# Performance work log

Measured on AMD Instinct MI355X. Metric: run time of the kernel, lower is better.

Reference implementation:

```python
import jax, jax.numpy as jnp
import numpy as np

N_NODES = 50000
N_EDGES = 1600000
E_DIM = 128
N_LAYERS = 3
N_GRAPHS = 32


def setup_inputs() -> dict:
    key = jax.random.key(0)
    ks = jax.random.split(key, 12)
    x = jax.random.normal(ks[0], (N_NODES,), dtype=jnp.float32)
    edge_index = jax.random.randint(ks[1], (2, N_EDGES), 0, N_NODES, dtype=jnp.int32)
    batch = jnp.sort(jax.random.randint(ks[2], (N_NODES,), 0, N_GRAPHS, dtype=jnp.int32))
    s_in = 1.0  # fan_in = 1 for the first linear
    s_e = 1.0 / np.sqrt(E_DIM)
    lin_w = jax.random.normal(ks[3], (1, E_DIM), jnp.float32) * s_in
    lin_b = jax.random.normal(ks[4], (E_DIM,), jnp.float32) * 0.01
    gcn_w = jax.random.normal(ks[5], (N_LAYERS, E_DIM, E_DIM), jnp.float32) * s_e
    gcn_b = jax.random.normal(ks[6], (N_LAYERS, E_DIM), jnp.float32) * 0.01
    r1_w = jax.random.normal(ks[7], (E_DIM, E_DIM), jnp.float32) * s_e
    r1_b = jax.random.normal(ks[8], (E_DIM,), jnp.float32) * 0.01
    r2_w = jax.random.normal(ks[9], (E_DIM, 1), jnp.float32) * s_e
    r2_b = jax.random.normal(ks[10], (1,), jnp.float32) * 0.01
    return {"x": x, "edge_index": edge_index, "batch": batch,
            "lin_w": lin_w, "lin_b": lin_b, "gcn_w": gcn_w, "gcn_b": gcn_b,
            "r1_w": r1_w, "r1_b": r1_b, "r2_w": r2_w, "r2_b": r2_b}


def reference(x, edge_index, batch, lin_w, lin_b, gcn_w, gcn_b, r1_w, r1_b, r2_w, r2_b):
    # input embedding: x.view(-1, 1) @ W + b -> [N, E]
    h = x.reshape(-1, 1) @ lin_w + lin_b

    # GCN normalization (add self-loops, symmetric deg^-1/2 norm) — structure is
    # identical across layers, so compute once.
    loops = jnp.arange(N_NODES, dtype=edge_index.dtype)
    src = jnp.concatenate([edge_index[0], loops])
    dst = jnp.concatenate([edge_index[1], loops])
    deg = jax.ops.segment_sum(jnp.ones(src.shape[0], h.dtype), dst, num_segments=N_NODES)
    dinv = jnp.where(deg > 0, jax.lax.rsqrt(deg), 0.0)
    norm = (dinv[src] * dinv[dst])[:, None]  # [E+N, 1]

    # NOTE: original calls x.relu() without assignment -> no activation (faithful).
    for l in range(N_LAYERS):
        h = h @ gcn_w[l]                                        # [N, E]
        h = jax.ops.segment_sum(h[src] * norm, dst, num_segments=N_NODES) + gcn_b[l]

    # global_add_pool over graphs
    pooled = jax.ops.segment_sum(h, batch, num_segments=N_GRAPHS)  # [G, E]
    hr = jnp.tanh(pooled @ r1_w + r1_b)
    return hr @ r2_w + r2_b  # [G, 1]
```

## Files before the change

kernel.cpp:

```cpp
#include <hip/hip_runtime.h>
#include <hip/hip_bf16.h>
#include <math.h>

#define NGRAPH 32
#define CAP 10240
#define EPT 24
#define EPB (256 * EPT)

__global__ void k_part(const int* __restrict__ src, const int* __restrict__ dst,
                       int* __restrict__ gcursor, unsigned int* __restrict__ packed, int E) {
    __shared__ unsigned int ldsbuf[EPB];
    __shared__ int hist[256], lofs[256], lcur[256], base[256];
    int tid = threadIdx.x;
    int e0 = blockIdx.x * EPB;
    hist[tid] = 0;
    __syncthreads();
    int d[EPT], s[EPT];
#pragma unroll
    for (int c = 0; c < EPT / 4; c++) {
        int e = e0 + c * 1024 + (tid << 2);
        if (e + 3 < E) {
            int4 dv = *(const int4*)&dst[e];
            int4 sv = *(const int4*)&src[e];
            d[4*c+0] = dv.x; d[4*c+1] = dv.y; d[4*c+2] = dv.z; d[4*c+3] = dv.w;
            s[4*c+0] = sv.x; s[4*c+1] = sv.y; s[4*c+2] = sv.z; s[4*c+3] = sv.w;
            atomicAdd(&hist[dv.x >> 8], 1);
            atomicAdd(&hist[dv.y >> 8], 1);
            atomicAdd(&hist[dv.z >> 8], 1);
            atomicAdd(&hist[dv.w >> 8], 1);
        } else {
#pragma unroll
            for (int k = 0; k < 4; k++) {
                int ee = e + k;
                if (ee < E) {
                    d[4*c+k] = dst[ee]; s[4*c+k] = src[ee];
                    atomicAdd(&hist[d[4*c+k] >> 8], 1);
                } else {
                    d[4*c+k] = -1;
                }
            }
        }
    }
    __syncthreads();
    int v = hist[tid];
    lofs[tid] = v;
    __syncthreads();
    for (int off = 1; off < 256; off <<= 1) {
        int t = (tid >= off) ? lofs[tid - off] : 0;
        __syncthreads();
        lofs[tid] += t;
        __syncthreads();
    }
    int total = lofs[255];
    int excl = lofs[tid] - v;
    lofs[tid] = excl;
    lcur[tid] = excl;
    if (v > 0) base[tid] = tid * CAP + atomicAdd(&gcursor[tid], v);
    __syncthreads();
#pragma unroll
    for (int c = 0; c < EPT; c++) {
        int dd = d[c];
        if (dd >= 0) {
            int bk = dd >> 8;
            int slot = atomicAdd(&lcur[bk], 1);
            ldsbuf[slot] = ((unsigned int)bk << 24) | ((unsigned int)s[c] << 8)
                         | (unsigned int)(dd & 255);
        }
    }
    __syncthreads();
    for (int i = tid; i < total; i += 256) {
        unsigned int w = ldsbuf[i];
        int bk = w >> 24;
        packed[base[bk] + (i - lofs[bk])] = w & 0xFFFFFFu;
    }
}

__global__ void k_bucket(const unsigned int* __restrict__ packed, const int* __restrict__ gcursor,
                         const float* __restrict__ x, const int* __restrict__ batch,
                         int* __restrict__ offs, int* __restrict__ deg,
                         float* __restrict__ dinv, float2* __restrict__ q0,
                         unsigned short* __restrict__ csr, float* __restrict__ S, int N) {
    __shared__ int cnt[256], lofs[256], lcur[256];
    __shared__ float cs[NGRAPH];
    int tid = threadIdx.x;
    int b = blockIdx.x;
    int start = b * CAP;
    int end = start + gcursor[b];
    cnt[tid] = 0;
    if (tid < NGRAPH) cs[tid] = 0.f;
    __syncthreads();
    for (int e = start + tid; e < end; e += 256)
        atomicAdd(&cnt[packed[e] & 255], 1);
    __syncthreads();
    int v = cnt[tid];
    lofs[tid] = v;
    __syncthreads();
    for (int off = 1; off < 256; off <<= 1) {
        int t = (tid >= off) ? lofs[tid - off] : 0;
        __syncthreads();
        lofs[tid] += t;
        __syncthreads();
    }
    int excl = lofs[tid] - v;
    lcur[tid] = excl;
    int node = b * 256 + tid;
    if (node < N) {
        deg[node] = v;
        offs[node] = start + excl;
        float dv = rsqrtf((float)(v + 1));
        dinv[node] = dv;
        q0[node] = make_float2(x[node] * dv, dv);
        atomicAdd(&cs[batch[node]], 1.f);
    }
    __syncthreads();
    for (int e = start + tid; e < end; e += 256) {
        unsigned int p = packed[e];
        int pos = start + atomicAdd(&lcur[p & 255], 1);
        csr[pos] = (unsigned short)(p >> 8);
    }
    if (tid < NGRAPH && cs[tid] != 0.f) atomicAdd(&S[tid], cs[tid]);
}

template <int WRITE_Q>
__global__ void k_hop(const float2* __restrict__ qin, float2* __restrict__ pout,
                      float2* __restrict__ qout, const unsigned short* __restrict__ csr,
                      const int* __restrict__ offs, const int* __restrict__ deg,
                      const float* __restrict__ dinv, int N) {
    int tid = threadIdx.x;
    int lane = tid & 15;
    int node = blockIdx.x * 16 + (tid >> 4);
    if (node >= N) return;
    int e = offs[node], ne = deg[node];
    float sx = 0.0f, su = 0.0f;
    int j = lane;
    for (; j + 16 < ne; j += 32) {
        int i0 = csr[e + j];
        int i1 = csr[e + j + 16];
        float2 a = qin[i0];
        float2 b = qin[i1];
        sx += a.x + b.x;
        su += a.y + b.y;
    }
    if (j < ne) {
        float2 a = qin[csr[e + j]];
        sx += a.x; su += a.y;
    }
#pragma unroll
    for (int m = 8; m > 0; m >>= 1) {
        sx += __shfl_xor(sx, m);
        su += __shfl_xor(su, m);
    }
    if (lane == 0) {
        float2 qs = qin[node];
        float dv = dinv[node];
        float px = dv * (sx + qs.x), pu = dv * (su + qs.y);
        pout[node] = make_float2(px, pu);
        if (WRITE_Q) qout[node] = make_float2(px * dv, pu * dv);
    }
}

__global__ void k_sums(const float2* __restrict__ p1, const float2* __restrict__ p2,
                       const float2* __restrict__ p3, const int* __restrict__ batch,
                       float* __restrict__ S, int N) {
    __shared__ float bins[4 * NGRAPH];
    int tid = threadIdx.x;
    if (tid < 4 * NGRAPH) bins[tid] = 0.f;
    __syncthreads();
    int i = blockIdx.x * 256 + tid;
    if (i < N) {
        int g = batch[i];
        atomicAdd(&bins[g], p1[i].y);
        atomicAdd(&bins[32 + g], p2[i].y);
        atomicAdd(&bins[64 + g], p3[i].y);
        atomicAdd(&bins[96 + g], p3[i].x);
    }
    __syncthreads();
    if (tid < 4 * NGRAPH && bins[tid] != 0.f) atomicAdd(&S[32 + tid], bins[tid]);
}

__global__ void k_mlp(const float* __restrict__ S,
                      const float* __restrict__ lin_w, const float* __restrict__ lin_b,
                      const float* __restrict__ gcn_w, const float* __restrict__ gcn_b,
                      const float* __restrict__ r1_w, const float* __restrict__ r1_b,
                      const float* __restrict__ r2_w, const float* __restrict__ r2_b,
                      float* __restrict__ out) {
    __shared__ float va[128], vb[128], vc[128], vd[128], pl[128], red[128];
    int j = threadIdx.x;
    int g = blockIdx.x;
    va[j] = lin_w[j];
    vb[j] = lin_b[j];
    vc[j] = gcn_b[j];
    vd[j] = gcn_b[128 + j];
    __syncthreads();
    for (int l = 0; l < 3; l++) {
        const float* W = gcn_w + l * 128 * 128;
        float na = 0.f, nb = 0.f, nc = 0.f, nd = 0.f;
        for (int k = 0; k < 128; k++) {
            float w = W[k * 128 + j];
            na += va[k] * w;
            nb += vb[k] * w;
            nc += vc[k] * w;
            nd += vd[k] * w;
        }
        __syncthreads();
        va[j] = na; vb[j] = nb;
        if (l >= 1) vc[j] = nc;
        if (l >= 2) vd[j] = nd;
        __syncthreads();
    }
    float cnt = S[g], su1 = S[32 + g], su2 = S[64 + g], su3 = S[96 + g], sv3 = S[128 + g];
    const float* b3 = gcn_b + 2 * 128;
    pl[j] = sv3 * va[j] + su3 * vb[j] + su2 * vc[j] + su1 * vd[j] + cnt * b3[j];
    __syncthreads();
    float acc = r1_b[j];
#pragma unroll 4
    for (int k = 0; k < 128; k++) acc += pl[k] * r1_w[k * 128 + j];
    red[j] = tanhf(acc) * r2_w[j];
    __syncthreads();
    for (int sft = 64; sft > 0; sft >>= 1) {
        if (j < sft) red[j] += red[j + sft];
        __syncthreads();
    }
    if (j == 0) out[g] = red[0] + r2_b[0];
}

extern "C" void kernel_launch(void* const* d_in, const int* in_sizes, int n_in,
                              void* d_out, int out_size, void* d_ws, size_t ws_size,
                              hipStream_t stream) {
    const float* x     = (const float*)d_in[0];
    const int*   eidx  = (const int*)d_in[1];
    const int*   batch = (const int*)d_in[2];
    const float* lin_w = (const float*)d_in[3];
    const float* lin_b = (const float*)d_in[4];
    const float* gcn_w = (const float*)d_in[5];
    const float* gcn_b = (const float*)d_in[6];
    const float* r1_w  = (const float*)d_in[7];
    const float* r1_b  = (const float*)d_in[8];
    const float* r2_w  = (const float*)d_in[9];
    const float* r2_b  = (const float*)d_in[10];

    const int N = in_sizes[0];
    const int E = in_sizes[1] / 2;
    const int* src = eidx;
    const int* dst = eidx + E;
    const int NB = (N + 255) / 256;

    char* w = (char*)d_ws;
    float2* q0      = (float2*)w; w += (size_t)N * 8;
    float2* q1      = (float2*)w; w += (size_t)N * 8;
    float2* q2      = (float2*)w; w += (size_t)N * 8;
    float2* p1      = (float2*)w; w += (size_t)N * 8;
    float2* p2      = (float2*)w; w += (size_t)N * 8;
    float2* p3      = (float2*)w; w += (size_t)N * 8;
    unsigned int* packed = (unsigned int*)w; w += (size_t)256 * CAP * 4;
    int*    offs    = (int*)w;    w += (size_t)N * 4;
    int*    deg     = (int*)w;    w += (size_t)N * 4;
    float*  dinv    = (float*)w;  w += (size_t)N * 4;
    int*    gcursor = (int*)w;    w += 256 * 4;
    float*  S       = (float*)w;  w += 160 * 4;
    unsigned short* csr = (unsigned short*)w; w += (size_t)256 * CAP * 2;

    hipMemsetAsync(gcursor, 0, 256 * 4 + 160 * 4, stream);

    k_part<<<(E + EPB - 1) / EPB, 256, 0, stream>>>(src, dst, gcursor, packed, E);
    k_bucket<<<NB, 256, 0, stream>>>(packed, gcursor, x, batch, offs, deg, dinv, q0, csr, S, N);

    int hop_blocks = (N + 15) / 16;
    k_hop<1><<<hop_blocks, 256, 0, stream>>>(q0, p1, q1, csr, offs, deg, dinv, N);
    k_hop<1><<<hop_blocks, 256, 0, stream>>>(q1, p2, q2, csr, offs, deg, dinv, N);
    k_hop<0><<<hop_blocks, 256, 0, stream>>>(q2, p3, (float2*)nullptr, csr, offs, deg, dinv, N);

    k_sums<<<NB, 256, 0, stream>>>(p1, p2, p3, batch, S, N);
    k_mlp<<<NGRAPH, 128, 0, stream>>>(S, lin_w, lin_b, gcn_w, gcn_b,
                                      r1_w, r1_b, r2_w, r2_b, (float*)d_out);
}
```

Measured before the change: 173.2 us.

## Fuse all stages into one cooperative persistent kernel with grid syncs

Replaces the seven separate launches and the memset with a single cooperative kernel of 256 blocks of 1024 threads, using grid.sync between phases. The CSR build is dropped: each hop reads bucketed packed edges directly and accumulates into per-node LDS slots with shared atomics. Per-graph pooling sums are folded into the hop phases, so the separate sums pass and the p buffers disappear. This removes launch gaps and the CSR scatter, but it adds grid-wide barriers, LDS atomic contention, and the risk of occupancy limits on cooperative launch with large blocks.

```diff
diff --git a/kernel.cpp b/kernel.cpp
--- a/kernel.cpp
+++ b/kernel.cpp
@@ -1,227 +1,221 @@
 #include <hip/hip_runtime.h>
-#include <hip/hip_bf16.h>
+#include <hip/hip_cooperative_groups.h>
 #include <math.h>
+
+namespace cg = cooperative_groups;
 
 #define NGRAPH 32
 #define CAP 10240
-#define EPT 24
-#define EPB (256 * EPT)
-
-__global__ void k_part(const int* __restrict__ src, const int* __restrict__ dst,
-                       int* __restrict__ gcursor, unsigned int* __restrict__ packed, int E) {
+#define BT 1024
+#define EPT 8
+#define EPB (BT * EPT)
+
+__global__ __launch_bounds__(BT, 4) void k_fused(
+    const int* __restrict__ src, const int* __restrict__ dst,
+    const float* __restrict__ x, const int* __restrict__ batch,
+    const float* __restrict__ lin_w, const float* __restrict__ lin_b,
+    const float* __restrict__ gcn_w, const float* __restrict__ gcn_b,
+    const float* __restrict__ r1_w, const float* __restrict__ r1_b,
+    const float* __restrict__ r2_w, const float* __restrict__ r2_b,
+    float* __restrict__ out,
+    unsigned int* __restrict__ packed, float* __restrict__ dinv,
+    float2* __restrict__ q0, float2* __restrict__ q1, float2* __restrict__ q2,
+    int* __restrict__ gcursor, float* __restrict__ S,
+    int N, int E)
+{
+    cg::grid_group grid = cg::this_grid();
     __shared__ unsigned int ldsbuf[EPB];
-    __shared__ int hist[256], lofs[256], lcur[256], base[256];
-    int tid = threadIdx.x;
-    int e0 = blockIdx.x * EPB;
-    hist[tid] = 0;
-    __syncthreads();
-    int d[EPT], s[EPT];
-#pragma unroll
-    for (int c = 0; c < EPT / 4; c++) {
-        int e = e0 + c * 1024 + (tid << 2);
-        if (e + 3 < E) {
-            int4 dv = *(const int4*)&dst[e];
-            int4 sv = *(const int4*)&src[e];
-            d[4*c+0] = dv.x; d[4*c+1] = dv.y; d[4*c+2] = dv.z; d[4*c+3] = dv.w;
-            s[4*c+0] = sv.x; s[4*c+1] = sv.y; s[4*c+2] = sv.z; s[4*c+3] = sv.w;
-            atomicAdd(&hist[dv.x >> 8], 1);
-            atomicAdd(&hist[dv.y >> 8], 1);
-            atomicAdd(&hist[dv.z >> 8], 1);
-            atomicAdd(&hist[dv.w >> 8], 1);
-        } else {
-#pragma unroll
-            for (int k = 0; k < 4; k++) {
-                int ee = e + k;
-                if (ee < E) {
-                    d[4*c+k] = dst[ee]; s[4*c+k] = src[ee];
-                    atomicAdd(&hist[d[4*c+k] >> 8], 1);
-                } else {
-                    d[4*c+k] = -1;
+    __shared__ int hist[256], lofs[256], lcur[256], basearr[256];
+    __shared__ float accx[256], accu[256];
+    __shared__ float bins[3 * NGRAPH];
+    __shared__ float va[128], vb[128], vc[128], vd[128], pl[128], red[128];
+
+    const int tid = threadIdx.x;
+    const int b = blockIdx.x;
+    const int NB = (N + 255) >> 8;
+    const int ntiles = (E + EPB - 1) / EPB;
+
+    if (b == 0) {
+        if (tid < 256) gcursor[tid] = 0;
+        else if (tid < 256 + 160) S[tid - 256] = 0.f;
+    }
+    grid.sync();
+
+    if (b < ntiles) {
+        int e0 = b * EPB;
+        if (tid < 256) hist[tid] = 0;
+        __syncthreads();
+        int dA[EPT], sA[EPT];
+#pragma unroll
+        for (int c = 0; c < EPT / 4; c++) {
+            int e = e0 + c * 4096 + (tid << 2);
+            if (e + 3 < E) {
+                int4 dv4 = *(const int4*)&dst[e];
+                int4 sv4 = *(const int4*)&src[e];
+                dA[4*c+0] = dv4.x; dA[4*c+1] = dv4.y; dA[4*c+2] = dv4.z; dA[4*c+3] = dv4.w;
+                sA[4*c+0] = sv4.x; sA[4*c+1] = sv4.y; sA[4*c+2] = sv4.z; sA[4*c+3] = sv4.w;
+                atomicAdd(&hist[dv4.x >> 8], 1);
+                atomicAdd(&hist[dv4.y >> 8], 1);
+                atomicAdd(&hist[dv4.z >> 8], 1);
+                atomicAdd(&hist[dv4.w >> 8], 1);
+            } else {
+#pragma unroll
+                for (int k = 0; k < 4; k++) {
+                    int ee = e + k;
+                    if (ee < E) {
+                        dA[4*c+k] = dst[ee]; sA[4*c+k] = src[ee];
+                        atomicAdd(&hist[dA[4*c+k] >> 8], 1);
+                    } else {
+                        dA[4*c+k] = -1;
+                    }
                 }
             }
         }
-    }
-    __syncthreads();
-    int v = hist[tid];
-    lofs[tid] = v;
-    __syncthreads();
-    for (int off = 1; off < 256; off <<= 1) {
-        int t = (tid >= off) ? lofs[tid - off] : 0;
-        __syncthreads();
-        lofs[tid] += t;
-        __syncthreads();
-    }
-    int total = lofs[255];
-    int excl = lofs[tid] - v;
-    lofs[tid] = excl;
-    lcur[tid] = excl;
-    if (v > 0) base[tid] = tid * CAP + atomicAdd(&gcursor[tid], v);
-    __syncthreads();
-#pragma unroll
-    for (int c = 0; c < EPT; c++) {
-        int dd = d[c];
-        if (dd >= 0) {
-            int bk = dd >> 8;
-            int slot = atomicAdd(&lcur[bk], 1);
-            ldsbuf[slot] = ((unsigned int)bk << 24) | ((unsigned int)s[c] << 8)
-                         | (unsigned int)(dd & 255);
-        }
-    }
-    __syncthreads();
-    for (int i = tid; i < total; i += 256) {
-        unsigned int w = ldsbuf[i];
-        int bk = w >> 24;
-        packed[base[bk] + (i - lofs[bk])] = w & 0xFFFFFFu;
-    }
-}
-
-__global__ void k_bucket(const unsigned int* __restrict__ packed, const int* __restrict__ gcursor,
-                         const float* __restrict__ x, const int* __restrict__ batch,
-                         int* __restrict__ offs, int* __restrict__ deg,
-                         float* __restrict__ dinv, float2* __restrict__ q0,
-                         unsigned short* __restrict__ csr, float* __restrict__ S, int N) {
-    __shared__ int cnt[256], lofs[256], lcur[256];
-    __shared__ float cs[NGRAPH];
-    int tid = threadIdx.x;
-    int b = blockIdx.x;
-    int start = b * CAP;
-    int end = start + gcursor[b];
-    cnt[tid] = 0;
-    if (tid < NGRAPH) cs[tid] = 0.f;
-    __syncthreads();
-    for (int e = start + tid; e < end; e += 256)
-        atomicAdd(&cnt[packed[e] & 255], 1);
-    __syncthreads();
-    int v = cnt[tid];
-    lofs[tid] = v;
-    __syncthreads();
-    for (int off = 1; off < 256; off <<= 1) {
-        int t = (tid >= off) ? lofs[tid - off] : 0;
-        __syncthreads();
-        lofs[tid] += t;
-        __syncthreads();
-    }
-    int excl = lofs[tid] - v;
-    lcur[tid] = excl;
-    int node = b * 256 + tid;
-    if (node < N) {
-        deg[node] = v;
-        offs[node] = start + excl;
-        float dv = rsqrtf((float)(v + 1));
-        dinv[node] = dv;
-        q0[node] = make_float2(x[node] * dv, dv);
-        atomicAdd(&cs[batch[node]], 1.f);
-    }
-    __syncthreads();
-    for (int e = start + tid; e < end; e += 256) {
-        unsigned int p = packed[e];
-        int pos = start + atomicAdd(&lcur[p & 255], 1);
-        csr[pos] = (unsigned short)(p >> 8);
-    }
-    if (tid < NGRAPH && cs[tid] != 0.f) atomicAdd(&S[tid], cs[tid]);
-}
-
-template <int WRITE_Q>
-__global__ void k_hop(const float2* __restrict__ qin, float2* __restrict__ pout,
-                      float2* __restrict__ qout, const unsigned short* __restrict__ csr,
-                      const int* __restrict__ offs, const int* __restrict__ deg,
-                      const float* __restrict__ dinv, int N) {
-    int tid = threadIdx.x;
-    int lane = tid & 15;
-    int node = blockIdx.x * 16 + (tid >> 4);
-    if (node >= N) return;
-    int e = offs[node], ne = deg[node];
-    float sx = 0.0f, su = 0.0f;
-    int j = lane;
-    for (; j + 16 < ne; j += 32) {
-        int i0 = csr[e + j];
-        int i1 = csr[e + j + 16];
-        float2 a = qin[i0];
-        float2 b = qin[i1];
-        sx += a.x + b.x;
-        su += a.y + b.y;
-    }
-    if (j < ne) {
-        float2 a = qin[csr[e + j]];
-        sx += a.x; su += a.y;
-    }
-#pragma unroll
-    for (int m = 8; m > 0; m >>= 1) {
-        sx += __shfl_xor(sx, m);
-        su += __shfl_xor(su, m);
-    }
-    if (lane == 0) {
-        float2 qs = qin[node];
-        float dv = dinv[node];
-        float px = dv * (sx + qs.x), pu = dv * (su + qs.y);
-        pout[node] = make_float2(px, pu);
-        if (WRITE_Q) qout[node] = make_float2(px * dv, pu * dv);
-    }
-}
-
-__global__ void k_sums(const float2* __restrict__ p1, const float2* __restrict__ p2,
-                       const float2* __restrict__ p3, const int* __restrict__ batch,
-                       float* __restrict__ S, int N) {
-    __shared__ float bins[4 * NGRAPH];
-    int tid = threadIdx.x;
-    if (tid < 4 * NGRAPH) bins[tid] = 0.f;
-    __syncthreads();
-    int i = blockIdx.x * 256 + tid;
-    if (i < N) {
-        int g = batch[i];
-        atomicAdd(&bins[g], p1[i].y);
-        atomicAdd(&bins[32 + g], p2[i].y);
-        atomicAdd(&bins[64 + g], p3[i].y);
-        atomicAdd(&bins[96 + g], p3[i].x);
-    }
-    __syncthreads();
-    if (tid < 4 * NGRAPH && bins[tid] != 0.f) atomicAdd(&S[32 + tid], bins[tid]);
-}
-
-__global__ void k_mlp(const float* __restrict__ S,
-                      const float* __restrict__ lin_w, const float* __restrict__ lin_b,
-                      const float* __restrict__ gcn_w, const float* __restrict__ gcn_b,
-                      const float* __restrict__ r1_w, const float* __restrict__ r1_b,
-                      const float* __restrict__ r2_w, const float* __restrict__ r2_b,
-                      float* __restrict__ out) {
-    __shared__ float va[128], vb[128], vc[128], vd[128], pl[128], red[128];
-    int j = threadIdx.x;
-    int g = blockIdx.x;
-    va[j] = lin_w[j];
-    vb[j] = lin_b[j];
-    vc[j] = gcn_b[j];
-    vd[j] = gcn_b[128 + j];
-    __syncthreads();
+        __syncthreads();
+        int v = 0;
+        if (tid < 256) { v = hist[tid]; lofs[tid] = v; }
+        __syncthreads();
+        for (int off = 1; off < 256; off <<= 1) {
+            int t = 0;
+            if (tid < 256 && tid >= off) t = lofs[tid - off];
+            __syncthreads();
+            if (tid < 256) lofs[tid] += t;
+            __syncthreads();
+        }
+        int total = lofs[255];
+        __syncthreads();
+        if (tid < 256) {
+            int excl = lofs[tid] - v;
+            lofs[tid] = excl;
+            lcur[tid] = excl;
+            if (v > 0) basearr[tid] = tid * CAP + atomicAdd(&gcursor[tid], v);
+        }
+        __syncthreads();
+#pragma unroll
+        for (int c = 0; c < EPT; c++) {
+            int dd = dA[c];
+            if (dd >= 0) {
+                int bk = dd >> 8;
+                int slot = atomicAdd(&lcur[bk], 1);
+                ldsbuf[slot] = ((unsigned int)bk << 24) | ((unsigned int)sA[c] << 8)
+                             | (unsigned int)(dd & 255);
+            }
+        }
+        __syncthreads();
+        for (int i = tid; i < total; i += BT) {
+            unsigned int wv = ldsbuf[i];
+            int bk = wv >> 24;
+            packed[basearr[bk] + (i - lofs[bk])] = wv & 0xFFFFFFu;
+        }
+    }
+    grid.sync();
+
+    if (b < NB) {
+        if (tid < 256) hist[tid] = 0;
+        if (tid < NGRAPH) bins[tid] = 0.f;
+        __syncthreads();
+        int start = b * CAP, end = start + gcursor[b];
+        for (int e = start + tid; e < end; e += BT)
+            atomicAdd(&hist[packed[e] & 255], 1);
+        __syncthreads();
+        if (tid < 256) {
+            int node = b * 256 + tid;
+            if (node < N) {
+                float dv = rsqrtf((float)(hist[tid] + 1));
+                dinv[node] = dv;
+                q0[node] = make_float2(x[node] * dv, dv);
+                atomicAdd(&bins[batch[node]], 1.f);
+            }
+        }
+        __syncthreads();
+        if (tid < NGRAPH && bins[tid] != 0.f) atomicAdd(&S[tid], bins[tid]);
+    }
+    grid.sync();
+
+#pragma unroll
     for (int l = 0; l < 3; l++) {
-        const float* W = gcn_w + l * 128 * 128;
-        float na = 0.f, nb = 0.f, nc = 0.f, nd = 0.f;
-        for (int k = 0; k < 128; k++) {
-            float w = W[k * 128 + j];
-            na += va[k] * w;
-            nb += vb[k] * w;
-            nc += vc[k] * w;
-            nd += vd[k] * w;
-        }
-        __syncthreads();
-        va[j] = na; vb[j] = nb;
-        if (l >= 1) vc[j] = nc;
-        if (l >= 2) vd[j] = nd;
-        __syncthreads();
-    }
-    float cnt = S[g], su1 = S[32 + g], su2 = S[64 + g], su3 = S[96 + g], sv3 = S[128 + g];
-    const float* b3 = gcn_b + 2 * 128;
-    pl[j] = sv3 * va[j] + su3 * vb[j] + su2 * vc[j] + su1 * vd[j] + cnt * b3[j];
-    __syncthreads();
-    float acc = r1_b[j];
+        if (b < NB) {
+            const float2* qin = (l == 0) ? q0 : (l == 1) ? q1 : q2;
+            float2* qout      = (l == 0) ? q1 : (l == 1) ? q2 : (float2*)nullptr;
+            if (tid < 256) { accx[tid] = 0.f; accu[tid] = 0.f; }
+            if (tid < 2 * NGRAPH) bins[tid] = 0.f;
+            __syncthreads();
+            int start = b * CAP, end = start + gcursor[b];
+            for (int e = start + tid; e < end; e += BT) {
+                unsigned int p = packed[e];
+                float2 q = qin[p >> 8];
+                atomicAdd(&accx[p & 255], q.x);
+                atomicAdd(&accu[p & 255], q.y);
+            }
+            __syncthreads();
+            if (tid < 256) {
+                int node = b * 256 + tid;
+                if (node < N) {
+                    float2 qs = qin[node];
+                    float dv = dinv[node];
+                    float px = dv * (accx[tid] + qs.x), pu = dv * (accu[tid] + qs.y);
+                    int g = batch[node];
+                    atomicAdd(&bins[g], pu);
+                    if (l < 2) qout[node] = make_float2(px * dv, pu * dv);
+                    else       atomicAdd(&bins[NGRAPH + g], px);
+                }
+            }
+            __syncthreads();
+            if (tid < NGRAPH) {
+                if (bins[tid] != 0.f) atomicAdd(&S[32 + 32 * l + tid], bins[tid]);
+                if (l == 2 && bins[NGRAPH + tid] != 0.f) atomicAdd(&S[128 + tid], bins[NGRAPH + tid]);
+            }
+        }
+        grid.sync();
+    }
+
+    if (b < NGRAPH) {
+        int j = tid;
+        if (j < 128) {
+            va[j] = lin_w[j];
+            vb[j] = lin_b[j];
+            vc[j] = gcn_b[j];
+            vd[j] = gcn_b[128 + j];
+        }
+        __syncthreads();
+        for (int l = 0; l < 3; l++) {
+            const float* W = gcn_w + l * 128 * 128;
+            float na = 0.f, nb = 0.f, nc = 0.f, nd = 0.f;
+            if (j < 128) {
+                for (int k = 0; k < 128; k++) {
+                    float wv = W[k * 128 + j];
+                    na += va[k] * wv;
+                    nb += vb[k] * wv;
+                    nc += vc[k] * wv;
+                    nd += vd[k] * wv;
+                }
+            }
+            __syncthreads();
+            if (j < 128) {
+                va[j] = na; vb[j] = nb;
+                if (l >= 1) vc[j] = nc;
+                if (l >= 2) vd[j] = nd;
+            }
+            __syncthreads();
+        }
+        float cnt = S[b], su1 = S[32 + b], su2 = S[64 + b], su3 = S[96 + b], sv3 = S[128 + b];
+        const float* b3 = gcn_b + 2 * 128;
+        if (j < 128)
+            pl[j] = sv3 * va[j] + su3 * vb[j] + su2 * vc[j] + su1 * vd[j] + cnt * b3[j];
+        __syncthreads();
+        if (j < 128) {
+            float acc = r1_b[j];
 #pragma unroll 4
-    for (int k = 0; k < 128; k++) acc += pl[k] * r1_w[k * 128 + j];
-    red[j] = tanhf(acc) * r2_w[j];
-    __syncthreads();
-    for (int sft = 64; sft > 0; sft >>= 1) {
-        if (j < sft) red[j] += red[j + sft];
-        __syncthreads();
-    }
-    if (j == 0) out[g] = red[0] + r2_b[0];
+            for (int k = 0; k < 128; k++) acc += pl[k] * r1_w[k * 128 + j];
+            red[j] = tanhf(acc) * r2_w[j];
+        }
+        __syncthreads();
+        for (int sft = 64; sft > 0; sft >>= 1) {
+            if (j < sft) red[j] += red[j + sft];
+            __syncthreads();
+        }
+        if (j == 0) out[b] = red[0] + r2_b[0];
+    }
 }
 
 extern "C" void kernel_launch(void* const* d_in, const int* in_sizes, int n_in,
@@ -239,38 +233,30 @@
     const float* r2_w  = (const float*)d_in[9];
     const float* r2_b  = (const float*)d_in[10];
 
-    const int N = in_sizes[0];
-    const int E = in_sizes[1] / 2;
+    int N = in_sizes[0];
+    int E = in_sizes[1] / 2;
     const int* src = eidx;
     const int* dst = eidx + E;
-    const int NB = (N + 255) / 256;
 
     char* w = (char*)d_ws;
     float2* q0      = (float2*)w; w += (size_t)N * 8;
     float2* q1      = (float2*)w; w += (size_t)N * 8;
     float2* q2      = (float2*)w; w += (size_t)N * 8;
-    float2* p1      = (float2*)w; w += (size_t)N * 8;
-    float2* p2      = (float2*)w; w += (size_t)N * 8;
-    float2* p3      = (float2*)w; w += (size_t)N * 8;
     unsigned int* packed = (unsigned int*)w; w += (size_t)256 * CAP * 4;
-    int*    offs    = (int*)w;    w += (size_t)N * 4;
-    int*    deg     = (int*)w;    w += (size_t)N * 4;
     float*  dinv    = (float*)w;  w += (size_t)N * 4;
     int*    gcursor = (int*)w;    w += 256 * 4;
     float*  S       = (float*)w;  w += 160 * 4;
-    unsigned short* csr = (unsigned short*)w; w += (size_t)256 * CAP * 2;
-
-    hipMemsetAsync(gcursor, 0, 256 * 4 + 160 * 4, stream);
-
-    k_part<<<(E + EPB - 1) / EPB, 256, 0, stream>>>(src, dst, gcursor, packed, E);
-    k_bucket<<<NB, 256, 0, stream>>>(packed, gcursor, x, batch, offs, deg, dinv, q0, csr, S, N);
-
-    int hop_blocks = (N + 15) / 16;
-    k_hop<1><<<hop_blocks, 256, 0, stream>>>(q0, p1, q1, csr, offs, deg, dinv, N);
-    k_hop<1><<<hop_blocks, 256, 0, stream>>>(q1, p2, q2, csr, offs, deg, dinv, N);
-    k_hop<0><<<hop_blocks, 256, 0, stream>>>(q2, p3, (float2*)nullptr, csr, offs, deg, dinv, N);
-
-    k_sums<<<NB, 256, 0, stream>>>(p1, p2, p3, batch, S, N);
-    k_mlp<<<NGRAPH, 128, 0, stream>>>(S, lin_w, lin_b, gcn_w, gcn_b,
-                                      r1_w, r1_b, r2_w, r2_b, (float*)d_out);
+
+    float* outp = (float*)d_out;
+
+    void* args[] = {
+        (void*)&src, (void*)&dst, (void*)&x, (void*)&batch,
+        (void*)&lin_w, (void*)&lin_b, (void*)&gcn_w, (void*)&gcn_b,
+        (void*)&r1_w, (void*)&r1_b, (void*)&r2_w, (void*)&r2_b,
+        (void*)&outp, (void*)&packed, (void*)&dinv,
+        (void*)&q0, (void*)&q1, (void*)&q2,
+        (void*)&gcursor, (void*)&S, (void*)&N, (void*)&E
+    };
+    hipLaunchCooperativeKernel((const void*)k_fused, dim3(256), dim3(BT),
+                               args, 0, stream);
 }
```

New measurement: 361.6 us. +108.8%, slower.
